# Optimization experiments

Hardware: AMD Instinct MI355X
Metric: run time of the kernel (lower is better)

The kernel has to match this reference:

```python
import jax, jax.numpy as jnp
import numpy as np

E = 640000   # n_edges
D = 128      # feature_dim
N = 40000    # n_dst_nodes


def setup_inputs() -> dict:
    key = jax.random.key(0)
    k1, k2, k3 = jax.random.split(key, 3)
    src_emb = jax.random.normal(k1, (E, D), dtype=jnp.float32)
    dst_idx = jax.random.randint(k2, (E,), 0, N, dtype=jnp.int64)
    # nn.Linear default init scale ~ 1/sqrt(fan_in)
    W = jax.random.normal(k3, (D, D), dtype=jnp.float32) / jnp.sqrt(jnp.float32(D))
    b = jnp.zeros((D,), dtype=jnp.float32)
    return {"src_emb": src_emb, "W": W, "b": b, "dst_idx": dst_idx, "n_nodes": N}


def reference(src_emb, W, b, dst_idx, n_nodes):
    # msg_e = relu(Linear(src_emb))  -- per-edge messages [E, D]
    msg = jax.nn.relu(jnp.einsum("ed,fd->ef", src_emb, W) + b)
    # update_all(copy_edge, max) == segment max over destination nodes [N, D]
    h_node = jax.ops.segment_max(msg, dst_idx, num_segments=n_nodes)
    return h_node
```

## Files before the change

### kernel.cpp

```cpp
#include <hip/hip_runtime.h>
#include <hip/hip_bf16.h>

#define E_EDGES 640000
#define DIM     128
#define N_NODES 40000

typedef __bf16 bf16x8 __attribute__((ext_vector_type(8)));
typedef float  floatx4 __attribute__((ext_vector_type(4)));

__global__ void prep_kernel(const float* __restrict__ W,
                            __bf16* __restrict__ Wsw,
                            int* __restrict__ out_i) {
    int tid = blockIdx.x * blockDim.x + threadIdx.x;
    if (tid < N_NODES * DIM) out_i[tid] = 0xFF800000;
    if (tid < 2048) {
        int lane = tid & 63;
        int kb   = (tid >> 6) & 3;
        int nb   = tid >> 8;
        int f    = nb * 16 + (lane & 15);
        int k0   = kb * 32 + ((lane >> 4) & 3) * 8;
        const float* wrow = W + f * DIM + k0;
        __bf16* o = Wsw + tid * 8;
#pragma unroll
        for (int j = 0; j < 8; ++j) o[j] = (__bf16)wrow[j];
    }
}

__global__ __launch_bounds__(256)
void gemm_atomic_kernel(const float* __restrict__ src,
                        const __bf16* __restrict__ Wsw,
                        const float* __restrict__ bias,
                        const int* __restrict__ dst,
                        int* __restrict__ out_i) {
    const int lane = threadIdx.x & 63;
    const int wave = threadIdx.x >> 6;
    const int q    = lane >> 4;
    const int n    = lane & 15;
    const int eb   = blockIdx.x * 64 + wave * 16;

    floatx4 acc[8];
#pragma unroll
    for (int nb = 0; nb < 8; ++nb) acc[nb] = (floatx4)(0.0f);

    const float* arow = src + (size_t)(eb + n) * DIM + q * 8;
    const bf16x8* Wf = (const bf16x8*)Wsw;

#pragma unroll
    for (int kb = 0; kb < 4; ++kb) {
        float4 a0 = *(const float4*)(arow + kb * 32);
        float4 a1 = *(const float4*)(arow + kb * 32 + 4);
        bf16x8 af;
        af[0] = (__bf16)a0.x; af[1] = (__bf16)a0.y;
        af[2] = (__bf16)a0.z; af[3] = (__bf16)a0.w;
        af[4] = (__bf16)a1.x; af[5] = (__bf16)a1.y;
        af[6] = (__bf16)a1.z; af[7] = (__bf16)a1.w;
#pragma unroll
        for (int nb = 0; nb < 8; ++nb) {
            bf16x8 bf = Wf[(nb * 4 + kb) * 64 + lane];
            acc[nb] = __builtin_amdgcn_mfma_f32_16x16x32_bf16(af, bf, acc[nb], 0, 0, 0);
        }
    }

    int nodes[4];
#pragma unroll
    for (int r = 0; r < 4; ++r) nodes[r] = dst[eb + q * 4 + r];
#pragma unroll
    for (int nb = 0; nb < 8; ++nb) {
        const int col = nb * 16 + n;
        const float bv = bias[col];
#pragma unroll
        for (int r = 0; r < 4; ++r) {
            float v = acc[nb][r] + bv;
            v = v > 0.0f ? v : 0.0f;
            atomicMax(out_i + (size_t)nodes[r] * DIM + col, __float_as_int(v));
        }
    }
}

extern "C" void kernel_launch(void* const* d_in, const int* in_sizes, int n_in,
                              void* d_out, int out_size, void* d_ws, size_t ws_size,
                              hipStream_t stream) {
    const float* src  = (const float*)d_in[0];
    const float* W    = (const float*)d_in[1];
    const float* bias = (const float*)d_in[2];
    const int*   dst  = (const int*)d_in[3];

    __bf16* Wsw  = (__bf16*)d_ws;
    int*    outi = (int*)d_out;

    prep_kernel<<<(N_NODES * DIM + 255) / 256, 256, 0, stream>>>(W, Wsw, outi);
    gemm_atomic_kernel<<<E_EDGES / 64, 256, 0, stream>>>(src, Wsw, bias, dst, outi);
}
```

Baseline: 563.1 us.

## Replace per-element atomic max with CSR sort and per-node segment reduction

Builds a CSR grouping of edges by destination using histogram, single-block scan, and scatter kernels, then runs one wave per node that gathers its edges, does the MFMA GEMM, and reduces the maximum in registers before one plain store. This removes the E*D global atomicMax traffic and applies bias and relu once per node instead of per edge. In exchange it adds three extra launches, a serial single-block scan, gathered rather than contiguous source rows, and partially filled 16-edge tiles for low-degree nodes (average degree is about 16). Nodes with no edges return early and keep the -inf fill from the prep kernel.

```diff
diff --git a/kernel.cpp b/kernel.cpp
--- a/kernel.cpp
+++ b/kernel.cpp
@@ -8,11 +8,19 @@
 typedef __bf16 bf16x8 __attribute__((ext_vector_type(8)));
 typedef float  floatx4 __attribute__((ext_vector_type(4)));
 
+#define WS_WSW     0
+#define WS_COUNTS  32768
+#define WS_OFFSETS 196608
+#define WS_CURSOR  360448
+#define WS_SORTED  524288
+
 __global__ void prep_kernel(const float* __restrict__ W,
                             __bf16* __restrict__ Wsw,
+                            int* __restrict__ counts,
                             int* __restrict__ out_i) {
     int tid = blockIdx.x * blockDim.x + threadIdx.x;
     if (tid < N_NODES * DIM) out_i[tid] = 0xFF800000;
+    if (tid < N_NODES) counts[tid] = 0;
     if (tid < 2048) {
         int lane = tid & 63;
         int kb   = (tid >> 6) & 3;
@@ -26,53 +34,125 @@
     }
 }
 
+__global__ void hist_kernel(const int* __restrict__ dst, int* __restrict__ counts) {
+    int e = blockIdx.x * blockDim.x + threadIdx.x;
+    if (e < E_EDGES) atomicAdd(&counts[dst[e]], 1);
+}
+
+#define SCAN_T 1024
+__global__ __launch_bounds__(SCAN_T)
+void scan_kernel(const int* __restrict__ counts,
+                 int* __restrict__ offsets,
+                 int* __restrict__ cursor) {
+    __shared__ int sm[SCAN_T];
+    __shared__ int s_carry;
+    int tid = threadIdx.x;
+    if (tid == 0) s_carry = 0;
+    __syncthreads();
+    for (int base = 0; base < N_NODES; base += SCAN_T) {
+        int i = base + tid;
+        int x = (i < N_NODES) ? counts[i] : 0;
+        sm[tid] = x;
+        __syncthreads();
+#pragma unroll
+        for (int off = 1; off < SCAN_T; off <<= 1) {
+            int v = (tid >= off) ? sm[tid - off] : 0;
+            __syncthreads();
+            sm[tid] += v;
+            __syncthreads();
+        }
+        int carry = s_carry;
+        int incl  = sm[tid];
+        if (i < N_NODES) {
+            int excl = incl - x + carry;
+            offsets[i] = excl;
+            cursor[i]  = excl;
+        }
+        __syncthreads();
+        if (tid == SCAN_T - 1) s_carry = carry + incl;
+        __syncthreads();
+    }
+    if (tid == 0) offsets[N_NODES] = s_carry;
+}
+
+__global__ void scatter_kernel(const int* __restrict__ dst,
+                               int* __restrict__ cursor,
+                               int* __restrict__ sorted) {
+    int e = blockIdx.x * blockDim.x + threadIdx.x;
+    if (e < E_EDGES) {
+        int pos = atomicAdd(&cursor[dst[e]], 1);
+        sorted[pos] = e;
+    }
+}
+
 __global__ __launch_bounds__(256)
-void gemm_atomic_kernel(const float* __restrict__ src,
-                        const __bf16* __restrict__ Wsw,
-                        const float* __restrict__ bias,
-                        const int* __restrict__ dst,
-                        int* __restrict__ out_i) {
+void gemm_csr_kernel(const float* __restrict__ src,
+                     const __bf16* __restrict__ Wsw,
+                     const float* __restrict__ bias,
+                     const int* __restrict__ offsets,
+                     const int* __restrict__ sorted,
+                     float* __restrict__ out) {
     const int lane = threadIdx.x & 63;
     const int wave = threadIdx.x >> 6;
-    const int q    = lane >> 4;
-    const int n    = lane & 15;
-    const int eb   = blockIdx.x * 64 + wave * 16;
+    const int node = blockIdx.x * 4 + wave;
+    if (node >= N_NODES) return;
+    const int q = lane >> 4;
+    const int n = lane & 15;
 
-    floatx4 acc[8];
-#pragma unroll
-    for (int nb = 0; nb < 8; ++nb) acc[nb] = (floatx4)(0.0f);
+    const int s = offsets[node];
+    const int e = offsets[node + 1];
+    if (s == e) return;
 
-    const float* arow = src + (size_t)(eb + n) * DIM + q * 8;
     const bf16x8* Wf = (const bf16x8*)Wsw;
 
+    float cmax[8];
 #pragma unroll
-    for (int kb = 0; kb < 4; ++kb) {
-        float4 a0 = *(const float4*)(arow + kb * 32);
-        float4 a1 = *(const float4*)(arow + kb * 32 + 4);
-        bf16x8 af;
-        af[0] = (__bf16)a0.x; af[1] = (__bf16)a0.y;
-        af[2] = (__bf16)a0.z; af[3] = (__bf16)a0.w;
-        af[4] = (__bf16)a1.x; af[5] = (__bf16)a1.y;
-        af[6] = (__bf16)a1.z; af[7] = (__bf16)a1.w;
+    for (int nb = 0; nb < 8; ++nb) cmax[nb] = -3.0e38f;
+
+    for (int t = s; t < e; t += 16) {
+        int ei  = t + n;
+        int eid = sorted[ei < e ? ei : e - 1];
+        const float* arow = src + (size_t)eid * DIM + q * 8;
+
+        floatx4 acc[8];
+#pragma unroll
+        for (int nb = 0; nb < 8; ++nb) acc[nb] = (floatx4)(0.0f);
+
+#pragma unroll
+        for (int kb = 0; kb < 4; ++kb) {
+            float4 a0 = *(const float4*)(arow + kb * 32);
+            float4 a1 = *(const float4*)(arow + kb * 32 + 4);
+            bf16x8 af;
+            af[0] = (__bf16)a0.x; af[1] = (__bf16)a0.y;
+            af[2] = (__bf16)a0.z; af[3] = (__bf16)a0.w;
+            af[4] = (__bf16)a1.x; af[5] = (__bf16)a1.y;
+            af[6] = (__bf16)a1.z; af[7] = (__bf16)a1.w;
+#pragma unroll
+            for (int nb = 0; nb < 8; ++nb) {
+                bf16x8 bf = Wf[(nb * 4 + kb) * 64 + lane];
+                acc[nb] = __builtin_amdgcn_mfma_f32_16x16x32_bf16(af, bf, acc[nb], 0, 0, 0);
+            }
+        }
 #pragma unroll
         for (int nb = 0; nb < 8; ++nb) {
-            bf16x8 bf = Wf[(nb * 4 + kb) * 64 + lane];
-            acc[nb] = __builtin_amdgcn_mfma_f32_16x16x32_bf16(af, bf, acc[nb], 0, 0, 0);
+            float m01 = acc[nb][0] > acc[nb][1] ? acc[nb][0] : acc[nb][1];
+            float m23 = acc[nb][2] > acc[nb][3] ? acc[nb][2] : acc[nb][3];
+            float m = m01 > m23 ? m01 : m23;
+            cmax[nb] = cmax[nb] > m ? cmax[nb] : m;
         }
     }
 
-    int nodes[4];
-#pragma unroll
-    for (int r = 0; r < 4; ++r) nodes[r] = dst[eb + q * 4 + r];
 #pragma unroll
     for (int nb = 0; nb < 8; ++nb) {
-        const int col = nb * 16 + n;
-        const float bv = bias[col];
-#pragma unroll
-        for (int r = 0; r < 4; ++r) {
-            float v = acc[nb][r] + bv;
-            v = v > 0.0f ? v : 0.0f;
-            atomicMax(out_i + (size_t)nodes[r] * DIM + col, __float_as_int(v));
+        float v = cmax[nb];
+        float o = __shfl_xor(v, 16);
+        v = v > o ? v : o;
+        o = __shfl_xor(v, 32);
+        v = v > o ? v : o;
+        if (q == 0) {
+            int col = nb * 16 + n;
+            float r = v + bias[col];
+            out[(size_t)node * DIM + col] = r > 0.0f ? r : 0.0f;
         }
     }
 }
@@ -85,9 +165,17 @@
     const float* bias = (const float*)d_in[2];
     const int*   dst  = (const int*)d_in[3];
 
-    __bf16* Wsw  = (__bf16*)d_ws;
-    int*    outi = (int*)d_out;
+    char* ws = (char*)d_ws;
+    __bf16* Wsw     = (__bf16*)(ws + WS_WSW);
+    int*    counts  = (int*)(ws + WS_COUNTS);
+    int*    offsets = (int*)(ws + WS_OFFSETS);
+    int*    cursor  = (int*)(ws + WS_CURSOR);
+    int*    sorted  = (int*)(ws + WS_SORTED);
+    float*  out     = (float*)d_out;
 
-    prep_kernel<<<(N_NODES * DIM + 255) / 256, 256, 0, stream>>>(W, Wsw, outi);
-    gemm_atomic_kernel<<<E_EDGES / 64, 256, 0, stream>>>(src, Wsw, bias, dst, outi);
+    prep_kernel<<<(N_NODES * DIM + 255) / 256, 256, 0, stream>>>(W, Wsw, counts, (int*)d_out);
+    hist_kernel<<<(E_EDGES + 255) / 256, 256, 0, stream>>>(dst, counts);
+    scan_kernel<<<1, SCAN_T, 0, stream>>>(counts, offsets, cursor);
+    scatter_kernel<<<(E_EDGES + 255) / 256, 256, 0, stream>>>(dst, cursor, sorted);
+    gemm_csr_kernel<<<(N_NODES + 3) / 4, 256, 0, stream>>>(src, Wsw, bias, offsets, sorted, out);
 }
```

Result: slower. 697.4 us (+23.8%).
